# Kernel tuning notes

Measured on AMD Instinct MI355X. Metric: run time of the kernel, lower is better.

The kernel has to match this reference:

```python
import jax, jax.numpy as jnp
import numpy as np

B, S, D, H = 4, 2048, 768, 12
DEPTH = D // H


def setup_inputs() -> dict:
    key = jax.random.key(0)
    ks = jax.random.split(key, 8)
    scale = 1.0 / np.sqrt(D)
    return {
        "v": jax.random.normal(ks[0], (B, S, D), jnp.float32),
        "k": jax.random.normal(ks[1], (B, S, D), jnp.float32),
        "q": jax.random.normal(ks[2], (B, S, D), jnp.float32),
        "wq": jax.random.normal(ks[3], (D, D), jnp.float32) * scale,
        "wk": jax.random.normal(ks[4], (D, D), jnp.float32) * scale,
        "wv": jax.random.normal(ks[5], (D, D), jnp.float32) * scale,
        "wo": jax.random.normal(ks[6], (D, D), jnp.float32) * scale,
        "bo": jax.random.normal(ks[7], (D,), jnp.float32) * 0.01,
    }


def _split_heads(x):
    # [B, S, D] -> [B, H, S, depth]
    return x.reshape(B, S, H, DEPTH).transpose(0, 2, 1, 3)


def reference(v, k, q, wq, wk, wv, wo, bo):
    # nn.Linear(bias=False): y = x @ W.T
    qh = _split_heads(q @ wq.T)
    kh = _split_heads(k @ wk.T)
    vh = _split_heads(v @ wv.T)
    # scaled dot-product attention (mask=None)
    logits = jnp.einsum("bhqd,bhkd->bhqk", qh, kh) / jnp.sqrt(
        jnp.asarray(DEPTH, jnp.float32)
    )
    attn = jax.nn.softmax(logits, axis=-1)  # [B, H, Sq, Sk]
    out = jnp.einsum("bhqk,bhkd->bhqd", attn, vh)
    concat = out.transpose(0, 2, 1, 3).reshape(B, S, D)
    return concat @ wo.T + bo
```

## Files before the change

### kernel.cpp

```cpp
#include <hip/hip_runtime.h>
#include <math.h>

#define BB 4
#define SS 2048
#define DD 768
#define HH 12
#define DEPTH 64
#define M_TOTAL (BB * SS)
#define WSZ (DD * DD)

typedef __attribute__((ext_vector_type(8))) short bf16x8;
typedef __attribute__((ext_vector_type(16))) float f32x16;
typedef __attribute__((ext_vector_type(4))) float f32x4;
typedef __attribute__((ext_vector_type(4))) unsigned short us4;
typedef __attribute__((ext_vector_type(2))) unsigned int u32x2;
typedef __attribute__((ext_vector_type(4))) unsigned int u32x4;

__device__ __forceinline__ unsigned short f2b(float f) {
  unsigned u = __builtin_bit_cast(unsigned, f);
  return (unsigned short)((u + 0x8000u) >> 16);
}

__device__ __forceinline__ unsigned pkrnd(float lo, float hi) {
  unsigned a = __builtin_bit_cast(unsigned, lo) + 0x8000u;
  unsigned b = __builtin_bit_cast(unsigned, hi) + 0x8000u;
  return __builtin_amdgcn_perm(b, a, 0x07060302);
}

__device__ __forceinline__ us4 f2b4(float a, float b, float c, float d) {
  unsigned lo = pkrnd(a, b), hi = pkrnd(c, d);
  us4 t;
  t.x = (unsigned short)lo; t.y = (unsigned short)(lo >> 16);
  t.z = (unsigned short)hi; t.w = (unsigned short)(hi >> 16);
  return t;
}

__device__ __forceinline__ unsigned cvtpk(float a, float b) {
  unsigned d;
  asm("v_cvt_pk_bf16_f32 %0, %1, %2" : "=v"(d) : "v"(a), "v"(b));
  return d;
}

__device__ __forceinline__ u32x2 permswap(unsigned a, unsigned b) {
  auto r = __builtin_amdgcn_permlane32_swap(a, b, false, false);
  u32x2 out;
  out.x = r[0];
  out.y = r[1];
  return out;
}

__device__ __forceinline__ float fexp2(float x) {
  return __builtin_amdgcn_exp2f(x);
}

__device__ __forceinline__ void gl16(const void* g, void* l) {
  __builtin_amdgcn_global_load_lds(
      (const __attribute__((address_space(1))) unsigned int*)g,
      (__attribute__((address_space(3))) unsigned int*)l, 16, 0, 0);
}

__global__ __launch_bounds__(256) void prep(
    const float* __restrict__ s0, const float* __restrict__ s1,
    const float* __restrict__ s2, const float* __restrict__ s3,
    const float* __restrict__ s4, const float* __restrict__ s5,
    const float* __restrict__ s6, unsigned short* __restrict__ d0,
    unsigned short* __restrict__ d1, unsigned short* __restrict__ d2,
    unsigned short* __restrict__ d3, unsigned short* __restrict__ d4,
    unsigned short* __restrict__ d5, unsigned short* __restrict__ d6) {
  const float* s;
  unsigned short* d;
  int n;
  switch (blockIdx.y) {
    case 0: s = s0; d = d0; n = M_TOTAL * DD; break;
    case 1: s = s1; d = d1; n = M_TOTAL * DD; break;
    case 2: s = s2; d = d2; n = M_TOTAL * DD; break;
    case 3: s = s3; d = d3; n = WSZ; break;
    case 4: s = s4; d = d4; n = WSZ; break;
    case 5: s = s5; d = d5; n = WSZ; break;
    default: s = s6; d = d6; n = WSZ; break;
  }
  int idx = (blockIdx.x * 256 + threadIdx.x) * 4;
  if (idx >= n) return;
  float4 f = *(const float4*)(s + idx);
  *(us4*)(d + idx) = f2b4(f.x, f.y, f.z, f.w);
}

__global__ __launch_bounds__(256) void proj_qkv(
    const unsigned short* __restrict__ qb, const unsigned short* __restrict__ kb,
    const unsigned short* __restrict__ vb, const unsigned short* __restrict__ wqb,
    const unsigned short* __restrict__ wkb, const unsigned short* __restrict__ wvb,
    unsigned short* __restrict__ QF, unsigned short* __restrict__ KF,
    unsigned short* __restrict__ VF) {
  const int mode = blockIdx.z;
  const unsigned short* X;
  const unsigned short* W;
  if (mode == 0) { X = qb; W = wqb; }
  else if (mode == 1) { X = kb; W = wkb; }
  else { X = vb; W = wvb; }

  __shared__ __align__(16) char sm[34816];
  unsigned short* As = (unsigned short*)sm;
  unsigned short* Bs = (unsigned short*)(sm + 8192);
  unsigned short* Ts = (unsigned short*)sm;

  const int tid = threadIdx.x;
  const int lane = tid & 63, w_ = tid >> 6;
  const int lr = lane & 15, quad = lane >> 4;
  const int wm = (w_ & 1) * 64, wn = (w_ >> 1) * 64;
  const int lin = blockIdx.y * 64 + blockIdx.x;
  const int nlin = (lin & 7) * 48 + (lin >> 3);
  const int m0 = (nlin / 6) * 128, n0 = (nlin % 6) * 128;
  const int grow = lane >> 2, gcol = (lane & 3) * 8;

  f32x4 acc[4][4];
#pragma unroll
  for (int mt = 0; mt < 4; ++mt)
#pragma unroll
    for (int nt = 0; nt < 4; ++nt) acc[mt][nt] = (f32x4){0.f, 0.f, 0.f, 0.f};

  for (int k0 = 0; k0 < DD; k0 += 32) {
    __syncthreads();
#pragma unroll
    for (int i = 0; i < 2; ++i) {
      int c = 4 * i + w_;
      int row = c * 16 + grow;
      gl16(X + (size_t)(m0 + row) * DD + k0 + gcol, (char*)As + c * 1024);
      gl16(W + (size_t)(n0 + row) * DD + k0 + gcol, (char*)Bs + c * 1024);
    }
    __syncthreads();

    bf16x8 af[4];
#pragma unroll
    for (int mt = 0; mt < 4; ++mt)
      af[mt] = *(const bf16x8*)&As[(wm + 16 * mt + lr) * 32 + 8 * quad];
#pragma unroll
    for (int nt = 0; nt < 4; ++nt) {
      bf16x8 bf = *(const bf16x8*)&Bs[(wn + 16 * nt + lr) * 32 + 8 * quad];
#pragma unroll
      for (int mt = 0; mt < 4; ++mt)
        acc[mt][nt] = __builtin_amdgcn_mfma_f32_16x16x32_bf16(af[mt], bf,
                                                              acc[mt][nt], 0, 0, 0);
    }
  }

  __syncthreads();

  const int b_ = m0 >> 11;
  const int hbase = n0 >> 6;
  const int sgbase = (m0 & 2047) >> 5;

  if (mode < 2) {
    const float osc = (mode == 0) ? 0.18033688011f : 1.0f;
#pragma unroll
    for (int mt = 0; mt < 4; ++mt)
#pragma unroll
      for (int nt = 0; nt < 4; ++nt) {
        int n = wn + 16 * nt + lr;
        int mb = wm + 16 * mt + 4 * quad;
#pragma unroll
        for (int r = 0; r < 4; ++r)
          Ts[(mb + r) * 136 + n] = f2b(acc[mt][nt][r] * osc);
      }
    __syncthreads();
    unsigned short* O = (mode == 0) ? QF : KF;
    const int ks = tid >> 6, lane2 = tid & 63;
    const int mrow = lane2 & 31, hb = lane2 >> 5;
#pragma unroll
    for (int c = 0; c < 8; ++c) {
      int hl = c >> 2, sblk = c & 3;
      int bh = b_ * HH + hbase + hl;
      bf16x8 vv = *(const bf16x8*)&Ts[(sblk * 32 + mrow) * 136 + hl * 64 +
                                      ks * 16 + hb * 8];
      *(bf16x8*)(O + ((size_t)bh * 64 + sgbase + sblk) * 2048 + tid * 8) = vv;
    }
  } else {
#pragma unroll
    for (int mt = 0; mt < 4; ++mt)
#pragma unroll
      for (int nt = 0; nt < 4; ++nt) {
        int n = wn + 16 * nt + lr;
        int mb = wm + 16 * mt + 4 * quad;
        *(us4*)&Ts[n * 136 + mb] =
            f2b4(acc[mt][nt][0], acc[mt][nt][1], acc[mt][nt][2], acc[mt][nt][3]);
      }
    __syncthreads();
    const int ntv = tid >> 7, ks2 = (tid >> 6) & 1, lane2 = tid & 63;
#pragma unroll
    for (int c = 0; c < 8; ++c) {
      int hl = c >> 2, sblk = c & 3;
      int bh = b_ * HH + hbase + hl;
      bf16x8 vv = *(const bf16x8*)&Ts[(hl * 64 + ntv * 32 + (lane2 & 31)) * 136 +
                                      sblk * 32 + ks2 * 16 + (lane2 >> 5) * 8];
      *(bf16x8*)(VF + ((size_t)bh * 64 + sgbase + sblk) * 2048 + tid * 8) = vv;
    }
  }
}

struct KV {
  bf16x8 k[4];
  bf16x8 v[4];
};

__global__ __launch_bounds__(256) void attn(
    const unsigned short* __restrict__ QF, const unsigned short* __restrict__ KF,
    const unsigned short* __restrict__ VF, unsigned short* __restrict__ cc) {
  __shared__ __align__(16) char smem[19200];
  float (*Osh)[64][36] = (float (*)[64][36])smem;
  float (*Ls)[2][32] = (float (*)[2][32])(smem + 18432);
  float (*Linv)[32] = (float (*)[32])(smem + 18944);

  const int tid = threadIdx.x;
  const int lane = tid & 63, w_ = tid >> 6;
  const int wq = w_ & 1, wk = w_ >> 1;
  const int m32 = lane & 31, h = lane >> 5;
  const int lin = blockIdx.y * 32 + blockIdx.x;
  const int nlin = (lin & 7) * 192 + (lin >> 3);
  const int bh = nlin >> 5;
  const int q0 = (nlin & 31) * 64;
  const size_t perbh = (size_t)SS * DEPTH;

  const unsigned short* qfb = QF + (size_t)bh * perbh;
  const unsigned short* kfb = KF + (size_t)bh * perbh + (size_t)wk * 2048 + lane * 8;
  const unsigned short* vfb = VF + (size_t)bh * perbh + (size_t)wk * 2048 + lane * 8;

  bf16x8 qf[4];
  {
    const unsigned short* p = qfb + (size_t)((q0 >> 5) + wq) * 2048 + lane * 8;
#pragma unroll
    for (int ks = 0; ks < 4; ++ks) qf[ks] = *(const bf16x8*)(p + ks * 512);
  }

  f32x16 o[2];
#pragma unroll
  for (int nt = 0; nt < 2; ++nt)
#pragma unroll
    for (int r = 0; r < 16; ++r) o[nt][r] = 0.f;
  float l_lane = 0.f;

#define LOADKV(tile, dst)                                                    \
  do {                                                                       \
    const unsigned short* kp_ = kfb + (size_t)(tile) * 4096;                 \
    const unsigned short* vp_ = vfb + (size_t)(tile) * 4096;                 \
    _Pragma("unroll") for (int x_ = 0; x_ < 4; ++x_) {                       \
      (dst).k[x_] = *(const bf16x8*)(kp_ + x_ * 512);                        \
      (dst).v[x_] = *(const bf16x8*)(vp_ + x_ * 512);                        \
    }                                                                        \
  } while (0)

#define TILECOMP(kv)                                                         \
  do {                                                                       \
    f32x16 st;                                                               \
    _Pragma("unroll") for (int r_ = 0; r_ < 16; ++r_) st[r_] = 0.f;          \
    __builtin_amdgcn_s_setprio(1);                                           \
    _Pragma("unroll") for (int ks_ = 0; ks_ < 4; ++ks_)                      \
        st = __builtin_amdgcn_mfma_f32_32x32x16_bf16((kv).k[ks_], qf[ks_],   \
                                                     st, 0, 0, 0);           \
    __builtin_amdgcn_s_setprio(0);                                           \
    float e_[16];                                                            \
    _Pragma("unroll") for (int r_ = 0; r_ < 16; ++r_) e_[r_] = fexp2(st[r_]);\
    _Pragma("unroll") for (int g_ = 0; g_ < 4; ++g_)                         \
        l_lane += (e_[4 * g_ + 0] + e_[4 * g_ + 1]) +                        \
                  (e_[4 * g_ + 2] + e_[4 * g_ + 3]);                         \
    unsigned w00 = cvtpk(e_[0], e_[1]), w01 = cvtpk(e_[2], e_[3]);           \
    unsigned w10 = cvtpk(e_[4], e_[5]), w11 = cvtpk(e_[6], e_[7]);           \
    unsigned w20 = cvtpk(e_[8], e_[9]), w21 = cvtpk(e_[10], e_[11]);         \
    unsigned w30 = cvtpk(e_[12], e_[13]), w31 = cvtpk(e_[14], e_[15]);       \
    u32x2 r0 = permswap(w00, w10);                                           \
    u32x2 r1 = permswap(w01, w11);                                           \
    u32x2 r2 = permswap(w20, w30);                                           \
    u32x2 r3 = permswap(w21, w31);                                           \
    u32x4 paw0, paw1;                                                        \
    paw0.x = r0.x; paw0.y = r1.x; paw0.z = r0.y; paw0.w = r1.y;              \
    paw1.x = r2.x; paw1.y = r3.x; paw1.z = r2.y; paw1.w = r3.y;              \
    bf16x8 pa0 = __builtin_bit_cast(bf16x8, paw0);                           \
    bf16x8 pa1 = __builtin_bit_cast(bf16x8, paw1);                           \
    __builtin_amdgcn_s_setprio(1);                                           \
    o[0] = __builtin_amdgcn_mfma_f32_32x32x16_bf16(pa0, (kv).v[0], o[0],     \
                                                   0, 0, 0);                 \
    o[1] = __builtin_amdgcn_mfma_f32_32x32x16_bf16(pa0, (kv).v[2], o[1],     \
                                                   0, 0, 0);                 \
    o[0] = __builtin_amdgcn_mfma_f32_32x32x16_bf16(pa1, (kv).v[1], o[0],     \
                                                   0, 0, 0);                 \
    o[1] = __builtin_amdgcn_mfma_f32_32x32x16_bf16(pa1, (kv).v[3], o[1],     \
                                                   0, 0, 0);                 \
    __builtin_amdgcn_s_setprio(0);                                           \
  } while (0)

  KV b0, b1;
  LOADKV(0, b0);
  for (int t = 0; t < 32; t += 2) {
    LOADKV(t + 1, b1);
    TILECOMP(b0);
    if (t + 2 < 32) LOADKV(t + 2, b0);
    TILECOMP(b1);
  }

  l_lane += __shfl_xor(l_lane, 32);
  if (h == 0) Ls[wq][wk][m32] = l_lane;
  __syncthreads();
  if (wk == 1) {
#pragma unroll
    for (int nt = 0; nt < 2; ++nt)
#pragma unroll
      for (int g = 0; g < 4; ++g) {
        float4 t = make_float4(o[nt][4 * g], o[nt][4 * g + 1], o[nt][4 * g + 2],
                               o[nt][4 * g + 3]);
        *(float4*)&Osh[wq][32 * nt + m32][8 * g + 4 * h] = t;
      }
  } else if (tid < 64) {
    int qq = tid & 31, ww = tid >> 5;
    Linv[ww][qq] = 1.f / (Ls[ww][0][qq] + Ls[ww][1][qq]);
  }
  __syncthreads();
  if (wk == 0) {
    const int b_ = bh / HH, h_ = bh % HH;
#pragma unroll
    for (int g = 0; g < 4; ++g) {
      float4 li = *(const float4*)&Linv[wq][8 * g + 4 * h];
      float lia[4] = {li.x, li.y, li.z, li.w};
#pragma unroll
      for (int nt = 0; nt < 2; ++nt) {
        float4 ot = *(const float4*)&Osh[wq][32 * nt + m32][8 * g + 4 * h];
        float oa[4] = {ot.x, ot.y, ot.z, ot.w};
#pragma unroll
        for (int r = 0; r < 4; ++r) {
          int qg = q0 + 32 * wq + 8 * g + 4 * h + r;
          float val = (o[nt][4 * g + r] + oa[r]) * lia[r];
          cc[((size_t)b_ * SS + qg) * DD + h_ * DEPTH + 32 * nt + m32] = f2b(val);
        }
      }
    }
  }
}

__global__ __launch_bounds__(256) void proj_out(
    const unsigned short* __restrict__ cc, const unsigned short* __restrict__ wob,
    const float* __restrict__ bo, float* __restrict__ out) {
  __shared__ __align__(16) unsigned short As[128 * 32];
  __shared__ __align__(16) unsigned short Bs[128 * 32];

  const int tid = threadIdx.x;
  const int lane = tid & 63, w_ = tid >> 6;
  const int lr = lane & 15, quad = lane >> 4;
  const int wm = (w_ & 1) * 64, wn = (w_ >> 1) * 64;
  const int lin = blockIdx.y * 64 + blockIdx.x;
  const int nlin = (lin & 7) * 48 + (lin >> 3);
  const int m0 = (nlin / 6) * 128, n0 = (nlin % 6) * 128;
  const int grow = lane >> 2, gcol = (lane & 3) * 8;

  f32x4 acc[4][4];
#pragma unroll
  for (int mt = 0; mt < 4; ++mt)
#pragma unroll
    for (int nt = 0; nt < 4; ++nt) acc[mt][nt] = (f32x4){0.f, 0.f, 0.f, 0.f};

  for (int k0 = 0; k0 < DD; k0 += 32) {
    __syncthreads();
#pragma unroll
    for (int i = 0; i < 2; ++i) {
      int c = 4 * i + w_;
      int row = c * 16 + grow;
      gl16(cc + (size_t)(m0 + row) * DD + k0 + gcol, (char*)As + c * 1024);
      gl16(wob + (size_t)(n0 + row) * DD + k0 + gcol, (char*)Bs + c * 1024);
    }
    __syncthreads();

    bf16x8 af[4];
#pragma unroll
    for (int mt = 0; mt < 4; ++mt)
      af[mt] = *(const bf16x8*)&As[(wm + 16 * mt + lr) * 32 + 8 * quad];
#pragma unroll
    for (int nt = 0; nt < 4; ++nt) {
      bf16x8 bf = *(const bf16x8*)&Bs[(wn + 16 * nt + lr) * 32 + 8 * quad];
#pragma unroll
      for (int mt = 0; mt < 4; ++mt)
        acc[mt][nt] = __builtin_amdgcn_mfma_f32_16x16x32_bf16(af[mt], bf,
                                                              acc[mt][nt], 0, 0, 0);
    }
  }

#pragma unroll
  for (int mt = 0; mt < 4; ++mt)
#pragma unroll
    for (int nt = 0; nt < 4; ++nt) {
      int n = n0 + wn + 16 * nt + lr;
      float bias = bo[n];
#pragma unroll
      for (int r = 0; r < 4; ++r) {
        int m = m0 + wm + 16 * mt + 4 * quad + r;
        out[(size_t)m * DD + n] = acc[mt][nt][r] + bias;
      }
    }
}

extern "C" void kernel_launch(void* const* d_in, const int* in_sizes, int n_in,
                              void* d_out, int out_size, void* d_ws,
                              size_t ws_size, hipStream_t stream) {
  const float* v = (const float*)d_in[0];
  const float* k = (const float*)d_in[1];
  const float* q = (const float*)d_in[2];
  const float* wq = (const float*)d_in[3];
  const float* wk = (const float*)d_in[4];
  const float* wv = (const float*)d_in[5];
  const float* wo = (const float*)d_in[6];
  const float* bo = (const float*)d_in[7];
  float* out = (float*)d_out;

  const size_t per = (size_t)BB * HH * SS * DEPTH;
  unsigned short* QF = (unsigned short*)d_ws;
  unsigned short* KF = QF + per;
  unsigned short* VF = KF + per;
  unsigned short* cc = VF + per;
  unsigned short* qb = cc + per;
  unsigned short* kb = qb + per;
  unsigned short* vb = kb + per;
  unsigned short* wqb = vb + per;
  unsigned short* wkb = wqb + WSZ;
  unsigned short* wvb = wkb + WSZ;
  unsigned short* wob = wvb + WSZ;

  dim3 g0(M_TOTAL * DD / 1024, 7);
  prep<<<g0, 256, 0, stream>>>(q, k, v, wq, wk, wv, wo, qb, kb, vb, wqb, wkb,
                               wvb, wob);

  dim3 g1(M_TOTAL / 128, DD / 128, 3);
  proj_qkv<<<g1, 256, 0, stream>>>(qb, kb, vb, wqb, wkb, wvb, QF, KF, VF);

  dim3 g2(SS / 64, BB * HH);
  attn<<<g2, 256, 0, stream>>>(QF, KF, VF, cc);

  dim3 g3(M_TOTAL / 128, DD / 128);
  proj_out<<<g3, 256, 0, stream>>>(cc, wob, bo, out);
}
```

Before: 273.5 us.

## Stage K/V tiles through triple-buffered LDS with direct global-to-LDS loads

```diff
diff --git a/kernel.cpp b/kernel.cpp
--- a/kernel.cpp
+++ b/kernel.cpp
@@ -196,18 +196,13 @@
   }
 }
 
-struct KV {
-  bf16x8 k[4];
-  bf16x8 v[4];
-};
-
 __global__ __launch_bounds__(256) void attn(
     const unsigned short* __restrict__ QF, const unsigned short* __restrict__ KF,
     const unsigned short* __restrict__ VF, unsigned short* __restrict__ cc) {
-  __shared__ __align__(16) char smem[19200];
+  __shared__ __align__(16) char smem[49920];
   float (*Osh)[64][36] = (float (*)[64][36])smem;
-  float (*Ls)[2][32] = (float (*)[2][32])(smem + 18432);
-  float (*Linv)[32] = (float (*)[32])(smem + 18944);
+  float (*Ls)[2][32] = (float (*)[2][32])(smem + 49152);
+  float (*Linv)[32] = (float (*)[32])(smem + 49664);
 
   const int tid = threadIdx.x;
   const int lane = tid & 63, w_ = tid >> 6;
@@ -220,8 +215,8 @@
   const size_t perbh = (size_t)SS * DEPTH;
 
   const unsigned short* qfb = QF + (size_t)bh * perbh;
-  const unsigned short* kfb = KF + (size_t)bh * perbh + (size_t)wk * 2048 + lane * 8;
-  const unsigned short* vfb = VF + (size_t)bh * perbh + (size_t)wk * 2048 + lane * 8;
+  const char* kbase = (const char*)(KF + (size_t)bh * perbh) + w_ * 2048 + lane * 16;
+  const char* vbase = (const char*)(VF + (size_t)bh * perbh) + w_ * 2048 + lane * 16;
 
   bf16x8 qf[4];
   {
@@ -237,23 +232,32 @@
     for (int r = 0; r < 16; ++r) o[nt][r] = 0.f;
   float l_lane = 0.f;
 
-#define LOADKV(tile, dst)                                                    \
+#define STAGE(T, B)                                                          \
   do {                                                                       \
-    const unsigned short* kp_ = kfb + (size_t)(tile) * 4096;                 \
-    const unsigned short* vp_ = vfb + (size_t)(tile) * 4096;                 \
+    const char* kg_ = kbase + (size_t)(T) * 8192;                            \
+    const char* vg_ = vbase + (size_t)(T) * 8192;                            \
+    char* kl_ = smem + (B) * 16384 + w_ * 2048;                              \
+    char* vl_ = smem + (B) * 16384 + 8192 + w_ * 2048;                       \
+    gl16(kg_, kl_);                                                          \
+    gl16(kg_ + 1024, kl_ + 1024);                                            \
+    gl16(vg_, vl_);                                                          \
+    gl16(vg_ + 1024, vl_ + 1024);                                            \
+  } while (0)
+
+#define TILE(B)                                                              \
+  do {                                                                       \
+    const char* kr_ = smem + (B) * 16384 + wk * 4096 + lane * 16;            \
+    const char* vr_ = smem + (B) * 16384 + 8192 + wk * 4096 + lane * 16;     \
+    bf16x8 kf_[4], vf_[4];                                                   \
     _Pragma("unroll") for (int x_ = 0; x_ < 4; ++x_) {                       \
-      (dst).k[x_] = *(const bf16x8*)(kp_ + x_ * 512);                        \
-      (dst).v[x_] = *(const bf16x8*)(vp_ + x_ * 512);                        \
+      kf_[x_] = *(const bf16x8*)(kr_ + x_ * 1024);                           \
+      vf_[x_] = *(const bf16x8*)(vr_ + x_ * 1024);                           \
     }                                                                        \
-  } while (0)
-
-#define TILECOMP(kv)                                                         \
-  do {                                                                       \
     f32x16 st;                                                               \
     _Pragma("unroll") for (int r_ = 0; r_ < 16; ++r_) st[r_] = 0.f;          \
     __builtin_amdgcn_s_setprio(1);                                           \
     _Pragma("unroll") for (int ks_ = 0; ks_ < 4; ++ks_)                      \
-        st = __builtin_amdgcn_mfma_f32_32x32x16_bf16((kv).k[ks_], qf[ks_],   \
+        st = __builtin_amdgcn_mfma_f32_32x32x16_bf16(kf_[ks_], qf[ks_],      \
                                                      st, 0, 0, 0);           \
     __builtin_amdgcn_s_setprio(0);                                           \
     float e_[16];                                                            \
@@ -275,24 +279,28 @@
     bf16x8 pa0 = __builtin_bit_cast(bf16x8, paw0);                           \
     bf16x8 pa1 = __builtin_bit_cast(bf16x8, paw1);                           \
     __builtin_amdgcn_s_setprio(1);                                           \
-    o[0] = __builtin_amdgcn_mfma_f32_32x32x16_bf16(pa0, (kv).v[0], o[0],     \
+    o[0] = __builtin_amdgcn_mfma_f32_32x32x16_bf16(pa0, vf_[0], o[0],        \
                                                    0, 0, 0);                 \
-    o[1] = __builtin_amdgcn_mfma_f32_32x32x16_bf16(pa0, (kv).v[2], o[1],     \
+    o[1] = __builtin_amdgcn_mfma_f32_32x32x16_bf16(pa0, vf_[2], o[1],        \
                                                    0, 0, 0);                 \
-    o[0] = __builtin_amdgcn_mfma_f32_32x32x16_bf16(pa1, (kv).v[1], o[0],     \
+    o[0] = __builtin_amdgcn_mfma_f32_32x32x16_bf16(pa1, vf_[1], o[0],        \
                                                    0, 0, 0);                 \
-    o[1] = __builtin_amdgcn_mfma_f32_32x32x16_bf16(pa1, (kv).v[3], o[1],     \
+    o[1] = __builtin_amdgcn_mfma_f32_32x32x16_bf16(pa1, vf_[3], o[1],        \
                                                    0, 0, 0);                 \
     __builtin_amdgcn_s_setprio(0);                                           \
   } while (0)
 
-  KV b0, b1;
-  LOADKV(0, b0);
-  for (int t = 0; t < 32; t += 2) {
-    LOADKV(t + 1, b1);
-    TILECOMP(b0);
-    if (t + 2 < 32) LOADKV(t + 2, b0);
-    TILECOMP(b1);
+  STAGE(0, 0);
+  STAGE(1, 1);
+  for (int t = 0; t < 32; ++t) {
+    if (t < 31)
+      asm volatile("s_waitcnt vmcnt(4)" ::: "memory");
+    else
+      asm volatile("s_waitcnt vmcnt(0)" ::: "memory");
+    __builtin_amdgcn_s_barrier();
+    __builtin_amdgcn_sched_barrier(0);
+    if (t + 2 < 32) STAGE(t + 2, (t + 2) % 3);
+    TILE(t % 3);
   }
 
   l_lane += __shfl_xor(l_lane, 32);
```

New measurement: 274.1 us. About the same (+0.2%).
